# Kernel optimization log

Measured on AMD Instinct MI355X. Metric: run time of the kernel, lower is better.

Reference implementation:

```python
import jax, jax.numpy as jnp
import numpy as np

B, L, D, H, DFF = 4, 2048, 1024, 16, 4096
DH = D // H
INF = 1e12


def setup_inputs() -> dict:
    key = jax.random.key(0)
    ks = jax.random.split(key, 20)
    s = lambda fan_in: 1.0 / np.sqrt(fan_in)
    inp = {
        'x': jax.random.normal(ks[0], (B, L, D), jnp.float32),
        'mask': jax.random.bernoulli(ks[1], 0.1, (B, 1, 1, L)),
        'wq': jax.random.normal(ks[2], (D, D), jnp.float32) * s(D),
        'bq': jnp.zeros((D,), jnp.float32),
        'wk': jax.random.normal(ks[3], (D, D), jnp.float32) * s(D),
        'bk': jnp.zeros((D,), jnp.float32),
        'wv': jax.random.normal(ks[4], (D, D), jnp.float32) * s(D),
        'bv': jnp.zeros((D,), jnp.float32),
        'wo': jax.random.normal(ks[5], (D, D), jnp.float32) * s(D),
        'bo': jnp.zeros((D,), jnp.float32),
        'w1': jax.random.normal(ks[6], (D, DFF), jnp.float32) * s(D),
        'b1': jnp.zeros((DFF,), jnp.float32),
        'w2': jax.random.normal(ks[7], (DFF, D), jnp.float32) * s(DFF),
        'b2': jnp.zeros((D,), jnp.float32),
        'g1': jnp.ones((D,), jnp.float32),
        'beta1': jnp.zeros((D,), jnp.float32),
        'g2': jnp.ones((D,), jnp.float32),
        'beta2': jnp.zeros((D,), jnp.float32),
    }
    return inp


def _layernorm(x, g, b, eps=1e-5):
    mu = jnp.mean(x, axis=-1, keepdims=True)
    var = jnp.mean(jnp.square(x - mu), axis=-1, keepdims=True)
    return (x - mu) * jax.lax.rsqrt(var + eps) * g + b


def reference(x, mask, wq, bq, wk, bk, wv, bv, wo, bo, w1, b1, w2, b2, g1, beta1, g2, beta2):
    # --- self attention ---
    def split_heads(t):  # [B,L,D] -> [B,H,L,DH]
        return t.reshape(B, L, H, DH).transpose(0, 2, 1, 3)

    Q = split_heads(x @ wq + bq)
    K = split_heads(x @ wk + bk)
    V = split_heads(x @ wv + bv)

    dots = jnp.einsum('bhqd,bhkd->bhqk', Q, K) / np.sqrt(DH)  # [B,H,L,L]
    dots = jnp.where(mask, -INF, dots)
    attn = jax.nn.softmax(dots, axis=-1)
    out = jnp.einsum('bhqk,bhkd->bhqd', attn, V)
    out = out.transpose(0, 2, 1, 3).reshape(B, L, D)
    out = out @ wo + bo

    x = _layernorm(x + out, g1, beta1)

    # --- feed forward ---
    h = jax.nn.relu(x @ w1 + b1)
    ff = h @ w2 + b2
    x = _layernorm(x + ff, g2, beta2)
    return x
```

## Files before the change

kernel.cpp:

```cpp
#include <hip/hip_runtime.h>
#include <hip/hip_bf16.h>

#define B_   4
#define L_   2048
#define D_   1024
#define H_   16
#define DH_  64
#define DFF_ 4096
#define M_   (B_ * L_)

typedef __attribute__((ext_vector_type(8))) short bf16x8;
typedef __attribute__((ext_vector_type(4))) float f32x4;

#define GLOAD16(gp, lp)                                                       \
  __builtin_amdgcn_global_load_lds(                                           \
      (const __attribute__((address_space(1))) unsigned int*)(gp),            \
      (__attribute__((address_space(3))) unsigned int*)(lp), 16, 0, 0)

#if __has_builtin(__builtin_amdgcn_exp2f)
#define EXP2F(x) __builtin_amdgcn_exp2f(x)
#else
#define EXP2F(x) exp2f(x)
#endif

__global__ void mask_mode_detect(const unsigned int* __restrict__ m,
                                 int* __restrict__ mode) {
  __shared__ int flags[2];
  if (threadIdx.x < 2) flags[threadIdx.x] = 0;
  __syncthreads();
  int nf32 = 0, n01 = 0;
  for (int i = threadIdx.x; i < 2048; i += 256) {
    unsigned w = m[i];
    if (w != 0u && w != 0x3f800000u) nf32 = 1;
    if (w > 1u) n01 = 1;
  }
  if (nf32) atomicOr(&flags[0], 1);
  if (n01)  atomicOr(&flags[1], 1);
  __syncthreads();
  if (threadIdx.x == 0)
    *mode = (!flags[0]) ? 0 : ((!flags[1]) ? 1 : 2);
}

__global__ void mask_prep(const void* __restrict__ m,
                          const int* __restrict__ mode_p,
                          float* __restrict__ out, int n) {
  int i = blockIdx.x * 256 + threadIdx.x;
  if (i >= n) return;
  int mode = *mode_p;
  bool mk;
  if (mode == 0)      mk = reinterpret_cast<const float*>(m)[i] != 0.f;
  else if (mode == 1) mk = reinterpret_cast<const int*>(m)[i] != 0;
  else                mk = reinterpret_cast<const unsigned char*>(m)[i] != 0;
  out[i] = mk ? -1e12f : 0.f;
}

__global__ void cvt_f32_bf16(const float4* __restrict__ in,
                             ushort4* __restrict__ out, int n4) {
  int i = blockIdx.x * 256 + threadIdx.x;
  if (i >= n4) return;
  float4 v = in[i];
  __hip_bfloat16 a = __float2bfloat16(v.x);
  __hip_bfloat16 b = __float2bfloat16(v.y);
  __hip_bfloat16 c = __float2bfloat16(v.z);
  __hip_bfloat16 d = __float2bfloat16(v.w);
  ushort4 o;
  o.x = *reinterpret_cast<unsigned short*>(&a);
  o.y = *reinterpret_cast<unsigned short*>(&b);
  o.z = *reinterpret_cast<unsigned short*>(&c);
  o.w = *reinterpret_cast<unsigned short*>(&d);
  out[i] = o;
}

__global__ void transpose_cvt(const float* __restrict__ W,
                              __hip_bfloat16* __restrict__ Wt, int K, int N) {
  __shared__ float t[32][33];
  const int n0 = blockIdx.x * 32, k0 = blockIdx.y * 32;
  const int tx = threadIdx.x, ty = threadIdx.y;
#pragma unroll
  for (int i = 0; i < 4; ++i)
    t[ty + i * 8][tx] = W[(size_t)(k0 + ty + i * 8) * N + n0 + tx];
  __syncthreads();
#pragma unroll
  for (int i = 0; i < 4; ++i)
    Wt[(size_t)(n0 + ty + i * 8) * K + k0 + tx] =
        __float2bfloat16(t[tx][ty + i * 8]);
}

__global__ void transpose_v(const __hip_bfloat16* __restrict__ Vin,
                            __hip_bfloat16* __restrict__ Vt) {
  __shared__ __hip_bfloat16 t[32][33];
  const int l0 = blockIdx.x * 32, d0 = blockIdx.y * 32, b = blockIdx.z;
  const int tx = threadIdx.x, ty = threadIdx.y;
#pragma unroll
  for (int i = 0; i < 4; ++i)
    t[ty + i * 8][tx] = Vin[(size_t)(b * L_ + l0 + ty + i * 8) * D_ + d0 + tx];
  __syncthreads();
#pragma unroll
  for (int i = 0; i < 4; ++i) {
    int d = d0 + ty + i * 8;
    Vt[(size_t)(b * D_ + d) * L_ + l0 + tx] = t[tx][ty + i * 8];
  }
}

#define STAGE8(matptr, ldsbase, tile, kh, rowbase)                            \
  {                                                                           \
    _Pragma("unroll")                                                         \
    for (int j_ = 0; j_ < 2; ++j_) {                                          \
      const int s_ = j_ * 512 + tid;                                          \
      const int row_ = s_ >> 2;                                               \
      const int q_ = (s_ & 3) ^ ((row_ >> 1) & 3);                            \
      GLOAD16(&matptr[(size_t)((rowbase) + row_) * K + (tile) * 64 +          \
                      (kh) * 32 + q_ * 8],                                    \
              (ldsbase) + (j_ * 512 + (w << 6)) * 16);                        \
    }                                                                         \
  }

#define PHASE8(bufoff, rh, ks, dovm, ...)                                     \
  {                                                                           \
    if ((rh) == 0) {                                                          \
      _Pragma("unroll")                                                       \
      for (int j = 0; j < 4; ++j) {                                           \
        const int br = wn * 64 + j * 16 + r16;                                \
        bfr[j] = *reinterpret_cast<const bf16x8*>(                            \
            ldsB + (bufoff) + (ks) * 16384 + br * 64 +                        \
            ((hi * 16) ^ (((br >> 1) & 3) << 4)));                            \
      }                                                                       \
    }                                                                         \
    bf16x8 af[4];                                                             \
    _Pragma("unroll")                                                         \
    for (int i = 0; i < 4; ++i) {                                             \
      const int ar = wm * 128 + (rh) * 64 + i * 16 + r16;                     \
      af[i] = *reinterpret_cast<const bf16x8*>(                               \
          ldsA + (bufoff) + (ks) * 16384 + ar * 64 +                          \
          ((hi * 16) ^ (((ar >> 1) & 3) << 4)));                              \
    }                                                                         \
    __VA_ARGS__;                                                              \
    __builtin_amdgcn_s_barrier();                                             \
    asm volatile("s_waitcnt lgkmcnt(0)" ::: "memory");                        \
    __builtin_amdgcn_sched_barrier(0);                                        \
    __builtin_amdgcn_s_setprio(1);                                            \
    _Pragma("unroll")                                                         \
    for (int i = 0; i < 4; ++i)                                               \
      _Pragma("unroll")                                                       \
      for (int j = 0; j < 4; ++j)                                             \
        acc[(rh) * 4 + i][j] = __builtin_amdgcn_mfma_f32_16x16x32_bf16(       \
            af[i], bfr[j], acc[(rh) * 4 + i][j], 0, 0, 0);                    \
    __builtin_amdgcn_s_setprio(0);                                            \
    if (dovm) {                                                               \
      asm volatile("s_waitcnt vmcnt(4)" ::: "memory");                        \
      __builtin_amdgcn_sched_barrier(0);                                      \
    }                                                                         \
    __builtin_amdgcn_s_barrier();                                             \
  }

template <int EP>
__global__ __launch_bounds__(512, 1) void gemm8(
    const __hip_bfloat16* __restrict__ A, const __hip_bfloat16* __restrict__ Bt,
    const float* __restrict__ bias, void* __restrict__ out,
    int M, int N, int K) {
  __shared__ __align__(16) char lds8[131072];
  char* const ldsA = lds8;
  char* const ldsB = lds8 + 65536;

  const int tid = threadIdx.x;
  const int lane = tid & 63;
  const int w = tid >> 6;
  const int wm = w >> 2;
  const int wn = w & 3;
  const int r16 = lane & 15;
  const int hi = lane >> 4;

  const int nwg = gridDim.x;
  const int orig = blockIdx.x;
  const int swz = (orig & 7) * (nwg >> 3) + (orig >> 3);
  const int bm = (swz & 31) * 256;
  const int bn = (swz >> 5) * 256;

  f32x4 acc[8][4];
#pragma unroll
  for (int i = 0; i < 8; ++i)
#pragma unroll
    for (int j = 0; j < 4; ++j) acc[i][j] = (f32x4){0.f, 0.f, 0.f, 0.f};
  bf16x8 bfr[4];

  const int nkt = K >> 6;
  const int nit = nkt >> 1;

  STAGE8(A, ldsA, 0, 0, bm);
  STAGE8(Bt, ldsB, 0, 0, bn);
  STAGE8(A, ldsA + 16384, 0, 1, bm);
  STAGE8(Bt, ldsB + 16384, 0, 1, bn);
  STAGE8(A, ldsA + 32768, 1, 0, bm);
  STAGE8(Bt, ldsB + 32768, 1, 0, bn);
  asm volatile("s_waitcnt vmcnt(4)" ::: "memory");
  __builtin_amdgcn_sched_barrier(0);
  __builtin_amdgcn_s_barrier();

  for (int it = 0; it < nit; ++it) {
    const int kt = it * 2;
    const bool hn = (it + 1) < nit;
    PHASE8(0, 0, 0, 0, STAGE8(A, ldsA + 49152, kt + 1, 1, bm));
    PHASE8(0, 1, 0, 0, STAGE8(Bt, ldsB + 49152, kt + 1, 1, bn));
    PHASE8(0, 0, 1, 0, if (hn) STAGE8(A, ldsA, kt + 2, 0, bm));
    PHASE8(0, 1, 1, 1, if (hn) STAGE8(Bt, ldsB, kt + 2, 0, bn));
    PHASE8(32768, 0, 0, 0, if (hn) STAGE8(A, ldsA + 16384, kt + 2, 1, bm));
    PHASE8(32768, 1, 0, 0, if (hn) STAGE8(Bt, ldsB + 16384, kt + 2, 1, bn));
    PHASE8(32768, 0, 1, 0, if (hn) STAGE8(A, ldsA + 32768, kt + 3, 0, bm));
    PHASE8(32768, 1, 1, 1, if (hn) STAGE8(Bt, ldsB + 32768, kt + 3, 0, bn));
  }

#pragma unroll
  for (int ri = 0; ri < 8; ++ri) {
#pragma unroll
    for (int j = 0; j < 4; ++j) {
      const int col = bn + wn * 64 + j * 16 + r16;
      const float bv = bias[col];
#pragma unroll
      for (int r = 0; r < 4; ++r) {
        const int row = bm + wm * 128 + ri * 16 + hi * 4 + r;
        const float v = acc[ri][j][r] + bv;
        if (EP == 1) {
          ((__hip_bfloat16*)out)[(size_t)row * N + col] =
              __float2bfloat16(v > 0.f ? v : 0.f);
        } else {
          __hip_bfloat16* outp =
              (__hip_bfloat16*)out + (size_t)(col >> 10) * (M_ * D_);
          outp[(size_t)row * 1024 + (col & 1023)] = __float2bfloat16(v);
        }
      }
    }
  }
}

template <int EP>
__global__ __launch_bounds__(256) void gemm_bt(
    const __hip_bfloat16* __restrict__ A, const __hip_bfloat16* __restrict__ Bt,
    const float* __restrict__ bias, const float* __restrict__ res,
    void* __restrict__ out, int M, int N, int K) {
  __shared__ __align__(16) char As[128 * 64];
  __shared__ __align__(16) char Bs[128 * 64];
  const int tid = threadIdx.x;
  const int lane = tid & 63;
  const int w = tid >> 6;
  const int wm = w >> 1, wn = w & 1;
  const int bm = blockIdx.x * 128;
  const int bn = blockIdx.y * 128;
  const int r16 = lane & 15;
  const int hi = lane >> 4;

  f32x4 acc[4][4];
#pragma unroll
  for (int m = 0; m < 4; ++m)
#pragma unroll
    for (int n = 0; n < 4; ++n) acc[m][n] = (f32x4){0.f, 0.f, 0.f, 0.f};

  for (int k0 = 0; k0 < K; k0 += 32) {
    __syncthreads();
#pragma unroll
    for (int c = 0; c < 2; ++c) {
      const int seg = c * 256 + tid;
      const int row = seg >> 2;
      const int csl = (seg & 3) ^ (row & 3);
      GLOAD16(&A[(size_t)(bm + row) * K + k0 + csl * 8],
              As + (c * 256 + w * 64) * 16);
      GLOAD16(&Bt[(size_t)(bn + row) * K + k0 + csl * 8],
              Bs + (c * 256 + w * 64) * 16);
    }
    __syncthreads();

    bf16x8 af[4], bfr[4];
#pragma unroll
    for (int m = 0; m < 4; ++m) {
      const int arow = wm * 64 + m * 16 + r16;
      af[m] = *reinterpret_cast<const bf16x8*>(
          As + arow * 64 + ((hi * 16) ^ ((arow & 3) << 4)));
    }
#pragma unroll
    for (int n = 0; n < 4; ++n) {
      const int brow = wn * 64 + n * 16 + r16;
      bfr[n] = *reinterpret_cast<const bf16x8*>(
          Bs + brow * 64 + ((hi * 16) ^ ((brow & 3) << 4)));
    }
#pragma unroll
    for (int m = 0; m < 4; ++m)
#pragma unroll
      for (int n = 0; n < 4; ++n)
        acc[m][n] = __builtin_amdgcn_mfma_f32_16x16x32_bf16(af[m], bfr[n],
                                                            acc[m][n], 0, 0, 0);
  }

  const int rg = hi * 4;
#pragma unroll
  for (int m = 0; m < 4; ++m) {
#pragma unroll
    for (int n = 0; n < 4; ++n) {
      const int col = bn + wn * 64 + n * 16 + r16;
      const float bv = bias[col];
#pragma unroll
      for (int r = 0; r < 4; ++r) {
        const int row = bm + wm * 64 + m * 16 + rg + r;
        const size_t idx = (size_t)row * N + col;
        float v = acc[m][n][r] + bv;
        if (EP == 0) {
          ((__hip_bfloat16*)out)[idx] = __float2bfloat16(v);
        } else if (EP == 1) {
          ((__hip_bfloat16*)out)[idx] = __float2bfloat16(v > 0.f ? v : 0.f);
        } else {
          ((float*)out)[idx] = v + res[idx];
        }
      }
    }
  }
}

__global__ __launch_bounds__(256) void attn_kernel(
    const __hip_bfloat16* __restrict__ Qg, const __hip_bfloat16* __restrict__ Kg,
    const __hip_bfloat16* __restrict__ VTg,
    const float* __restrict__ maskf,
    __hip_bfloat16* __restrict__ Og) {
  __shared__ __align__(16) char Kl[64 * 128];
  __shared__ __align__(16) char Vl[64 * 128];
  __shared__ __align__(16) char Pl[4][32 * 128];
  __shared__ float maskb[64];

  const int tid = threadIdx.x;
  const int lane = tid & 63;
  const int w = tid >> 6;
  const int hi = lane >> 4;
  const int r16 = lane & 15;
  const int swzk = (r16 & 7) << 4;

  const int nwg = gridDim.x;
  const int orig = blockIdx.x;
  const int swb = (orig & 7) * (nwg >> 3) + (orig >> 3);
  const int qb = swb & 15;
  const int bh = swb >> 4;
  const int b = bh >> 4;
  const int h = bh & 15;
  const int qbase = qb * 128 + w * 32;

  const float C = 0.18033688011112042f;

  bf16x8 qf[2][2];
#pragma unroll
  for (int m = 0; m < 2; ++m)
#pragma unroll
    for (int ks = 0; ks < 2; ++ks)
      qf[m][ks] = *reinterpret_cast<const bf16x8*>(
          &Qg[(size_t)(b * L_ + qbase + m * 16 + r16) * D_ + h * DH_ +
              ks * 32 + hi * 8]);

  float mrun[2] = {-1e30f, -1e30f};
  float lrun[2] = {0.f, 0.f};
  f32x4 o[2][4];
#pragma unroll
  for (int m = 0; m < 2; ++m)
#pragma unroll
    for (int nd = 0; nd < 4; ++nd) o[m][nd] = (f32x4){0.f, 0.f, 0.f, 0.f};

  char* const Plw = Pl[w];

  for (int kv0 = 0; kv0 < L_; kv0 += 64) {
    __syncthreads();
#pragma unroll
    for (int c = 0; c < 2; ++c) {
      const int seg = c * 256 + tid;
      const int row = seg >> 3;
      const int csl = (seg & 7) ^ (row & 7);
      GLOAD16(&Kg[(size_t)(b * L_ + kv0 + row) * D_ + h * DH_ + csl * 8],
              Kl + (c * 256 + w * 64) * 16);
      GLOAD16(&VTg[(size_t)(b * D_ + h * DH_ + row) * L_ + kv0 + csl * 8],
              Vl + (c * 256 + w * 64) * 16);
    }
    if (tid < 64) maskb[tid] = maskf[(size_t)b * L_ + kv0 + tid];
    __syncthreads();

    f32x4 sacc[2][4];
#pragma unroll
    for (int m = 0; m < 2; ++m)
#pragma unroll
      for (int n = 0; n < 4; ++n) sacc[m][n] = (f32x4){0.f, 0.f, 0.f, 0.f};
    __builtin_amdgcn_s_setprio(1);
#pragma unroll
    for (int n = 0; n < 4; ++n) {
      const int krow = n * 16 + r16;
#pragma unroll
      for (int ks = 0; ks < 2; ++ks) {
        const bf16x8 kf = *reinterpret_cast<const bf16x8*>(
            Kl + krow * 128 + ((ks * 64 + hi * 16) ^ swzk));
#pragma unroll
        for (int m = 0; m < 2; ++m)
          sacc[m][n] = __builtin_amdgcn_mfma_f32_16x16x32_bf16(
              kf, qf[m][ks], sacc[m][n], 0, 0, 0);
      }
    }
    __builtin_amdgcn_s_setprio(0);

#pragma unroll
    for (int m = 0; m < 2; ++m) {
      float p[4][4];
#pragma unroll
      for (int n = 0; n < 4; ++n) {
        const float4 mv =
            *reinterpret_cast<const float4*>(&maskb[n * 16 + hi * 4]);
        p[n][0] = fmaf(sacc[m][n][0], C, mv.x);
        p[n][1] = fmaf(sacc[m][n][1], C, mv.y);
        p[n][2] = fmaf(sacc[m][n][2], C, mv.z);
        p[n][3] = fmaf(sacc[m][n][3], C, mv.w);
      }
      float lm = p[0][0];
#pragma unroll
      for (int n = 0; n < 4; ++n)
#pragma unroll
        for (int r = 0; r < 4; ++r) lm = fmaxf(lm, p[n][r]);
      lm = fmaxf(lm, __shfl_xor(lm, 16, 64));
      lm = fmaxf(lm, __shfl_xor(lm, 32, 64));
      if (!__all(lm <= mrun[m] + 8.f)) {
        const float mn = fmaxf(mrun[m], lm);
        const float corr = EXP2F(mrun[m] - mn);
        mrun[m] = mn;
        lrun[m] *= corr;
        float crs[4];
#pragma unroll
        for (int r = 0; r < 4; ++r)
          crs[r] = __shfl(corr, (lane & 48) | (hi * 4 + r), 64);
#pragma unroll
        for (int nd = 0; nd < 4; ++nd)
#pragma unroll
          for (int r = 0; r < 4; ++r) o[m][nd][r] *= crs[r];
      }
      const float mr = mrun[m];
      float ls = 0.f;
      const int prow = m * 16 + r16;
#pragma unroll
      for (int n = 0; n < 4; ++n) {
        union { unsigned long long u; unsigned short us[4]; } pk;
#pragma unroll
        for (int r = 0; r < 4; ++r) {
          const float e = EXP2F(p[n][r] - mr);
          ls += e;
          __hip_bfloat16 t = __float2bfloat16(e);
          pk.us[r] = *reinterpret_cast<unsigned short*>(&t);
        }
        *reinterpret_cast<unsigned long long*>(
            Plw + prow * 128 + ((n * 32 + hi * 8) ^ swzk)) = pk.u;
      }
      lrun[m] += ls;
    }

    bf16x8 pa[2][2];
#pragma unroll
    for (int m = 0; m < 2; ++m)
#pragma unroll
      for (int ks = 0; ks < 2; ++ks)
        pa[m][ks] = *reinterpret_cast<const bf16x8*>(
            Plw + (m * 16 + r16) * 128 + ((ks * 64 + hi * 16) ^ swzk));
    __builtin_amdgcn_s_setprio(1);
#pragma unroll
    for (int nd = 0; nd < 4; ++nd) {
      const int vrow = nd * 16 + r16;
#pragma unroll
      for (int ks = 0; ks < 2; ++ks) {
        const bf16x8 vb = *reinterpret_cast<const bf16x8*>(
            Vl + vrow * 128 + ((ks * 64 + hi * 16) ^ swzk));
#pragma unroll
        for (int m = 0; m < 2; ++m)
          o[m][nd] = __builtin_amdgcn_mfma_f32_16x16x32_bf16(pa[m][ks], vb,
                                                             o[m][nd], 0, 0, 0);
      }
    }
    __builtin_amdgcn_s_setprio(0);
  }

#pragma unroll
  for (int m = 0; m < 2; ++m) {
    lrun[m] += __shfl_xor(lrun[m], 16, 64);
    lrun[m] += __shfl_xor(lrun[m], 32, 64);
    const float inv = 1.f / lrun[m];
    float invr[4];
#pragma unroll
    for (int r = 0; r < 4; ++r)
      invr[r] = __shfl(inv, (lane & 48) | (hi * 4 + r), 64);
#pragma unroll
    for (int r = 0; r < 4; ++r) {
      const int q = qbase + m * 16 + hi * 4 + r;
#pragma unroll
      for (int nd = 0; nd < 4; ++nd)
        Og[(size_t)(b * L_ + q) * D_ + h * DH_ + nd * 16 + r16] =
            __float2bfloat16(o[m][nd][r] * invr[r]);
    }
  }
}

__global__ __launch_bounds__(256) void layernorm_kernel(
    const float* __restrict__ in, const float* __restrict__ g,
    const float* __restrict__ be, float* __restrict__ outf,
    __hip_bfloat16* __restrict__ outb) {
  const int row = blockIdx.x;
  const int tid = threadIdx.x;
  const float4 v = reinterpret_cast<const float4*>(in + (size_t)row * D_)[tid];
  float s = v.x + v.y + v.z + v.w;
  float ss = v.x * v.x + v.y * v.y + v.z * v.z + v.w * v.w;
#pragma unroll
  for (int off = 1; off < 64; off <<= 1) {
    s += __shfl_xor(s, off, 64);
    ss += __shfl_xor(ss, off, 64);
  }
  __shared__ float red[8];
  const int w = tid >> 6, lane = tid & 63;
  if (lane == 0) { red[w] = s; red[4 + w] = ss; }
  __syncthreads();
  s = red[0] + red[1] + red[2] + red[3];
  ss = red[4] + red[5] + red[6] + red[7];
  const float mu = s * (1.f / D_);
  const float rs = rsqrtf(ss * (1.f / D_) - mu * mu + 1e-5f);
  const float4 gv = reinterpret_cast<const float4*>(g)[tid];
  const float4 bv = reinterpret_cast<const float4*>(be)[tid];
  float4 ov;
  ov.x = (v.x - mu) * rs * gv.x + bv.x;
  ov.y = (v.y - mu) * rs * gv.y + bv.y;
  ov.z = (v.z - mu) * rs * gv.z + bv.z;
  ov.w = (v.w - mu) * rs * gv.w + bv.w;
  reinterpret_cast<float4*>(outf + (size_t)row * D_)[tid] = ov;
  if (outb) {
    __hip_bfloat16 t[4] = {__float2bfloat16(ov.x), __float2bfloat16(ov.y),
                           __float2bfloat16(ov.z), __float2bfloat16(ov.w)};
    *reinterpret_cast<uint2*>(&outb[(size_t)row * D_ + tid * 4]) =
        *reinterpret_cast<const uint2*>(t);
  }
}

extern "C" void kernel_launch(void* const* d_in, const int* in_sizes, int n_in,
                              void* d_out, int out_size, void* d_ws,
                              size_t ws_size, hipStream_t stream) {
  (void)in_sizes; (void)n_in; (void)out_size; (void)ws_size;
  const float* x   = (const float*)d_in[0];
  const void*  msk = d_in[1];
  const float* wq  = (const float*)d_in[2];
  const float* bq  = (const float*)d_in[3];
  const float* wk  = (const float*)d_in[4];
  const float* bk  = (const float*)d_in[5];
  const float* wv  = (const float*)d_in[6];
  const float* bv  = (const float*)d_in[7];
  const float* wo  = (const float*)d_in[8];
  const float* bo  = (const float*)d_in[9];
  const float* w1  = (const float*)d_in[10];
  const float* b1  = (const float*)d_in[11];
  const float* w2  = (const float*)d_in[12];
  const float* b2  = (const float*)d_in[13];
  const float* g1  = (const float*)d_in[14];
  const float* be1 = (const float*)d_in[15];
  const float* g2  = (const float*)d_in[16];
  const float* be2 = (const float*)d_in[17];

  char* ws = (char*)d_ws;
  int*            MODE  = (int*)(ws + 0);
  float*          MASKF = (float*)(ws + 256);
  float*          BIASC = (float*)(ws + 40960);
  __hip_bfloat16* XB    = (__hip_bfloat16*)(ws + 65536);
  __hip_bfloat16* WQT   = (__hip_bfloat16*)(ws + 16842752);
  __hip_bfloat16* WKT   = (__hip_bfloat16*)(ws + 18939904);
  __hip_bfloat16* WVT   = (__hip_bfloat16*)(ws + 21037056);
  __hip_bfloat16* WOT   = (__hip_bfloat16*)(ws + 23134208);
  __hip_bfloat16* W1T   = (__hip_bfloat16*)(ws + 25231360);
  __hip_bfloat16* W2T   = (__hip_bfloat16*)(ws + 33619968);
  __hip_bfloat16* QB    = (__hip_bfloat16*)(ws + 42008576);
  __hip_bfloat16* KB    = (__hip_bfloat16*)(ws + 58785792);
  __hip_bfloat16* VB    = (__hip_bfloat16*)(ws + 75563008);
  __hip_bfloat16* OB    = (__hip_bfloat16*)(ws + 92340224);
  __hip_bfloat16* HB    = QB;
  __hip_bfloat16* VT    = (__hip_bfloat16*)(ws + 109117440);
  float*          R1    = (float*)(ws + 125894656);
  float*          OUT   = (float*)d_out;

  mask_mode_detect<<<1, 256, 0, stream>>>((const unsigned int*)msk, MODE);
  mask_prep<<<(B_ * L_ + 255) / 256, 256, 0, stream>>>(msk, MODE, MASKF, B_ * L_);
  cvt_f32_bf16<<<(M_ * D_ / 4 + 255) / 256, 256, 0, stream>>>(
      (const float4*)x, (ushort4*)XB, M_ * D_ / 4);
  hipMemcpyAsync(BIASC, bq, D_ * 4, hipMemcpyDeviceToDevice, stream);
  hipMemcpyAsync(BIASC + D_, bk, D_ * 4, hipMemcpyDeviceToDevice, stream);
  hipMemcpyAsync(BIASC + 2 * D_, bv, D_ * 4, hipMemcpyDeviceToDevice, stream);

  dim3 tb(32, 8);
  transpose_cvt<<<dim3(D_ / 32, D_ / 32), tb, 0, stream>>>(wq, WQT, D_, D_);
  transpose_cvt<<<dim3(D_ / 32, D_ / 32), tb, 0, stream>>>(wk, WKT, D_, D_);
  transpose_cvt<<<dim3(D_ / 32, D_ / 32), tb, 0, stream>>>(wv, WVT, D_, D_);
  transpose_cvt<<<dim3(D_ / 32, D_ / 32), tb, 0, stream>>>(wo, WOT, D_, D_);
  transpose_cvt<<<dim3(DFF_ / 32, D_ / 32), tb, 0, stream>>>(w1, W1T, D_, DFF_);
  transpose_cvt<<<dim3(D_ / 32, DFF_ / 32), tb, 0, stream>>>(w2, W2T, DFF_, D_);

  gemm8<3><<<dim3((M_ / 256) * (3 * D_ / 256)), 512, 0, stream>>>(
      XB, WQT, BIASC, QB, M_, 3 * D_, D_);

  transpose_v<<<dim3(L_ / 32, D_ / 32, B_), tb, 0, stream>>>(VB, VT);
  attn_kernel<<<dim3(B_ * H_ * (L_ / 128)), 256, 0, stream>>>(QB, KB, VT, MASKF, OB);

  gemm_bt<2><<<dim3(M_ / 128, D_ / 128), 256, 0, stream>>>(OB, WOT, bo, x, R1, M_, D_, D_);
  layernorm_kernel<<<M_, 256, 0, stream>>>(R1, g1, be1, R1, XB);
  gemm8<1><<<dim3((M_ / 256) * (DFF_ / 256)), 512, 0, stream>>>(
      XB, W1T, b1, HB, M_, DFF_, D_);
  gemm_bt<2><<<dim3(M_ / 128, D_ / 128), 256, 0, stream>>>(HB, W2T, b2, R1, OUT, M_, D_, DFF_);
  layernorm_kernel<<<M_, 256, 0, stream>>>(OUT, g2, be2, OUT, nullptr);
}
```

Measured before the change: 490.1 us.

## Split-K the FFN down-projection on the large GEMM kernel and fuse combine with LayerNorm

The second FFN GEMM (K=4096, N=1024) now runs on the 256x256 gemm8 kernel with a 2-way split over K, which gives 256 workgroups instead of 128. Each half writes an fp32 partial, and a new combine_ln2 kernel sums both partials with the residual and bias before applying LayerNorm. This replaces the smaller 128-tile gemm_bt plus a separate layernorm pass. The attention row-max reduction is also rewritten as a tree. The cost is about 64MB of extra fp32 partial traffic, and the path only runs if the workspace is large enough.

```diff
diff --git a/kernel.cpp b/kernel.cpp
--- a/kernel.cpp
+++ b/kernel.cpp
@@ -102,14 +102,14 @@
   }
 }
 
-#define STAGE8(matptr, ldsbase, tile, kh, rowbase)                            \
+#define STAGE8(matptr, stride, ldsbase, tile, kh, rowbase)                    \
   {                                                                           \
     _Pragma("unroll")                                                         \
     for (int j_ = 0; j_ < 2; ++j_) {                                          \
       const int s_ = j_ * 512 + tid;                                          \
       const int row_ = s_ >> 2;                                               \
       const int q_ = (s_ & 3) ^ ((row_ >> 1) & 3);                            \
-      GLOAD16(&matptr[(size_t)((rowbase) + row_) * K + (tile) * 64 +          \
+      GLOAD16(&matptr[(size_t)((rowbase) + row_) * (stride) + (tile) * 64 +   \
                       (kh) * 32 + q_ * 8],                                    \
               (ldsbase) + (j_ * 512 + (w << 6)) * 16);                        \
     }                                                                         \
@@ -157,7 +157,7 @@
 __global__ __launch_bounds__(512, 1) void gemm8(
     const __hip_bfloat16* __restrict__ A, const __hip_bfloat16* __restrict__ Bt,
     const float* __restrict__ bias, void* __restrict__ out,
-    int M, int N, int K) {
+    int M, int N, int K, int lda, int ldb) {
   __shared__ __align__(16) char lds8[131072];
   char* const ldsA = lds8;
   char* const ldsB = lds8 + 65536;
@@ -173,8 +173,21 @@
   const int nwg = gridDim.x;
   const int orig = blockIdx.x;
   const int swz = (orig & 7) * (nwg >> 3) + (orig >> 3);
-  const int bm = (swz & 31) * 256;
-  const int bn = (swz >> 5) * 256;
+
+  int bm, bn, kh = 0;
+  const __hip_bfloat16* Ap = A;
+  const __hip_bfloat16* Bp = Bt;
+  if (EP == 4) {
+    kh = swz & 1;
+    const int rest = swz >> 1;
+    bm = (rest & 31) * 256;
+    bn = (rest >> 5) * 256;
+    Ap += (size_t)kh * K;
+    Bp += (size_t)kh * K;
+  } else {
+    bm = (swz & 31) * 256;
+    bn = (swz >> 5) * 256;
+  }
 
   f32x4 acc[8][4];
 #pragma unroll
@@ -186,12 +199,12 @@
   const int nkt = K >> 6;
   const int nit = nkt >> 1;
 
-  STAGE8(A, ldsA, 0, 0, bm);
-  STAGE8(Bt, ldsB, 0, 0, bn);
-  STAGE8(A, ldsA + 16384, 0, 1, bm);
-  STAGE8(Bt, ldsB + 16384, 0, 1, bn);
-  STAGE8(A, ldsA + 32768, 1, 0, bm);
-  STAGE8(Bt, ldsB + 32768, 1, 0, bn);
+  STAGE8(Ap, lda, ldsA, 0, 0, bm);
+  STAGE8(Bp, ldb, ldsB, 0, 0, bn);
+  STAGE8(Ap, lda, ldsA + 16384, 0, 1, bm);
+  STAGE8(Bp, ldb, ldsB + 16384, 0, 1, bn);
+  STAGE8(Ap, lda, ldsA + 32768, 1, 0, bm);
+  STAGE8(Bp, ldb, ldsB + 32768, 1, 0, bn);
   asm volatile("s_waitcnt vmcnt(4)" ::: "memory");
   __builtin_amdgcn_sched_barrier(0);
   __builtin_amdgcn_s_barrier();
@@ -199,14 +212,14 @@
   for (int it = 0; it < nit; ++it) {
     const int kt = it * 2;
     const bool hn = (it + 1) < nit;
-    PHASE8(0, 0, 0, 0, STAGE8(A, ldsA + 49152, kt + 1, 1, bm));
-    PHASE8(0, 1, 0, 0, STAGE8(Bt, ldsB + 49152, kt + 1, 1, bn));
-    PHASE8(0, 0, 1, 0, if (hn) STAGE8(A, ldsA, kt + 2, 0, bm));
-    PHASE8(0, 1, 1, 1, if (hn) STAGE8(Bt, ldsB, kt + 2, 0, bn));
-    PHASE8(32768, 0, 0, 0, if (hn) STAGE8(A, ldsA + 16384, kt + 2, 1, bm));
-    PHASE8(32768, 1, 0, 0, if (hn) STAGE8(Bt, ldsB + 16384, kt + 2, 1, bn));
-    PHASE8(32768, 0, 1, 0, if (hn) STAGE8(A, ldsA + 32768, kt + 3, 0, bm));
-    PHASE8(32768, 1, 1, 1, if (hn) STAGE8(Bt, ldsB + 32768, kt + 3, 0, bn));
+    PHASE8(0, 0, 0, 0, STAGE8(Ap, lda, ldsA + 49152, kt + 1, 1, bm));
+    PHASE8(0, 1, 0, 0, STAGE8(Bp, ldb, ldsB + 49152, kt + 1, 1, bn));
+    PHASE8(0, 0, 1, 0, if (hn) STAGE8(Ap, lda, ldsA, kt + 2, 0, bm));
+    PHASE8(0, 1, 1, 1, if (hn) STAGE8(Bp, ldb, ldsB, kt + 2, 0, bn));
+    PHASE8(32768, 0, 0, 0, if (hn) STAGE8(Ap, lda, ldsA + 16384, kt + 2, 1, bm));
+    PHASE8(32768, 1, 0, 0, if (hn) STAGE8(Bp, ldb, ldsB + 16384, kt + 2, 1, bn));
+    PHASE8(32768, 0, 1, 0, if (hn) STAGE8(Ap, lda, ldsA + 32768, kt + 3, 0, bm));
+    PHASE8(32768, 1, 1, 1, if (hn) STAGE8(Bp, ldb, ldsB + 32768, kt + 3, 0, bn));
   }
 
 #pragma unroll
@@ -214,7 +227,7 @@
 #pragma unroll
     for (int j = 0; j < 4; ++j) {
       const int col = bn + wn * 64 + j * 16 + r16;
-      const float bv = bias[col];
+      const float bv = (EP == 4) ? 0.f : bias[col];
 #pragma unroll
       for (int r = 0; r < 4; ++r) {
         const int row = bm + wm * 128 + ri * 16 + hi * 4 + r;
@@ -222,10 +235,13 @@
         if (EP == 1) {
           ((__hip_bfloat16*)out)[(size_t)row * N + col] =
               __float2bfloat16(v > 0.f ? v : 0.f);
-        } else {
+        } else if (EP == 3) {
           __hip_bfloat16* outp =
               (__hip_bfloat16*)out + (size_t)(col >> 10) * (M_ * D_);
           outp[(size_t)row * 1024 + (col & 1023)] = __float2bfloat16(v);
+        } else {
+          float* outp = (float*)out + (size_t)kh * ((size_t)M * N);
+          outp[(size_t)row * N + col] = v;
         }
       }
     }
@@ -408,11 +424,11 @@
         p[n][2] = fmaf(sacc[m][n][2], C, mv.z);
         p[n][3] = fmaf(sacc[m][n][3], C, mv.w);
       }
-      float lm = p[0][0];
-#pragma unroll
-      for (int n = 0; n < 4; ++n)
-#pragma unroll
-        for (int r = 0; r < 4; ++r) lm = fmaxf(lm, p[n][r]);
+      float q0 = fmaxf(fmaxf(p[0][0], p[0][1]), fmaxf(p[0][2], p[0][3]));
+      float q1 = fmaxf(fmaxf(p[1][0], p[1][1]), fmaxf(p[1][2], p[1][3]));
+      float q2 = fmaxf(fmaxf(p[2][0], p[2][1]), fmaxf(p[2][2], p[2][3]));
+      float q3 = fmaxf(fmaxf(p[3][0], p[3][1]), fmaxf(p[3][2], p[3][3]));
+      float lm = fmaxf(fmaxf(q0, q1), fmaxf(q2, q3));
       lm = fmaxf(lm, __shfl_xor(lm, 16, 64));
       lm = fmaxf(lm, __shfl_xor(lm, 32, 64));
       if (!__all(lm <= mrun[m] + 8.f)) {
@@ -530,10 +546,51 @@
   }
 }
 
+__global__ __launch_bounds__(256) void combine_ln2(
+    const float* __restrict__ P0, const float* __restrict__ P1,
+    const float* __restrict__ res, const float* __restrict__ b2,
+    const float* __restrict__ g, const float* __restrict__ be,
+    float* __restrict__ out) {
+  const int row = blockIdx.x;
+  const int tid = threadIdx.x;
+  const float4 a = reinterpret_cast<const float4*>(P0 + (size_t)row * D_)[tid];
+  const float4 b = reinterpret_cast<const float4*>(P1 + (size_t)row * D_)[tid];
+  const float4 rr = reinterpret_cast<const float4*>(res + (size_t)row * D_)[tid];
+  const float4 bb = reinterpret_cast<const float4*>(b2)[tid];
+  float4 v;
+  v.x = a.x + b.x + rr.x + bb.x;
+  v.y = a.y + b.y + rr.y + bb.y;
+  v.z = a.z + b.z + rr.z + bb.z;
+  v.w = a.w + b.w + rr.w + bb.w;
+  float s = v.x + v.y + v.z + v.w;
+  float ss = v.x * v.x + v.y * v.y + v.z * v.z + v.w * v.w;
+#pragma unroll
+  for (int off = 1; off < 64; off <<= 1) {
+    s += __shfl_xor(s, off, 64);
+    ss += __shfl_xor(ss, off, 64);
+  }
+  __shared__ float red[8];
+  const int w = tid >> 6, lane = tid & 63;
+  if (lane == 0) { red[w] = s; red[4 + w] = ss; }
+  __syncthreads();
+  s = red[0] + red[1] + red[2] + red[3];
+  ss = red[4] + red[5] + red[6] + red[7];
+  const float mu = s * (1.f / D_);
+  const float rs = rsqrtf(ss * (1.f / D_) - mu * mu + 1e-5f);
+  const float4 gv = reinterpret_cast<const float4*>(g)[tid];
+  const float4 bv = reinterpret_cast<const float4*>(be)[tid];
+  float4 ov;
+  ov.x = (v.x - mu) * rs * gv.x + bv.x;
+  ov.y = (v.y - mu) * rs * gv.y + bv.y;
+  ov.z = (v.z - mu) * rs * gv.z + bv.z;
+  ov.w = (v.w - mu) * rs * gv.w + bv.w;
+  reinterpret_cast<float4*>(out + (size_t)row * D_)[tid] = ov;
+}
+
 extern "C" void kernel_launch(void* const* d_in, const int* in_sizes, int n_in,
                               void* d_out, int out_size, void* d_ws,
                               size_t ws_size, hipStream_t stream) {
-  (void)in_sizes; (void)n_in; (void)out_size; (void)ws_size;
+  (void)in_sizes; (void)n_in; (void)out_size;
   const float* x   = (const float*)d_in[0];
   const void*  msk = d_in[1];
   const float* wq  = (const float*)d_in[2];
@@ -571,7 +628,10 @@
   __hip_bfloat16* HB    = QB;
   __hip_bfloat16* VT    = (__hip_bfloat16*)(ws + 109117440);
   float*          R1    = (float*)(ws + 125894656);
+  float*          P0    = (float*)(ws + 159449088);
+  float*          P1    = (float*)(ws + 193003520);
   float*          OUT   = (float*)d_out;
+  const bool use_splitk = ws_size >= 226557952ull;
 
   mask_mode_detect<<<1, 256, 0, stream>>>((const unsigned int*)msk, MODE);
   mask_prep<<<(B_ * L_ + 255) / 256, 256, 0, stream>>>(msk, MODE, MASKF, B_ * L_);
@@ -590,7 +650,7 @@
   transpose_cvt<<<dim3(D_ / 32, DFF_ / 32), tb, 0, stream>>>(w2, W2T, DFF_, D_);
 
   gemm8<3><<<dim3((M_ / 256) * (3 * D_ / 256)), 512, 0, stream>>>(
-      XB, WQT, BIASC, QB, M_, 3 * D_, D_);
+      XB, WQT, BIASC, QB, M_, 3 * D_, D_, D_, D_);
 
   transpose_v<<<dim3(L_ / 32, D_ / 32, B_), tb, 0, stream>>>(VB, VT);
   attn_kernel<<<dim3(B_ * H_ * (L_ / 128)), 256, 0, stream>>>(QB, KB, VT, MASKF, OB);
@@ -598,7 +658,13 @@
   gemm_bt<2><<<dim3(M_ / 128, D_ / 128), 256, 0, stream>>>(OB, WOT, bo, x, R1, M_, D_, D_);
   layernorm_kernel<<<M_, 256, 0, stream>>>(R1, g1, be1, R1, XB);
   gemm8<1><<<dim3((M_ / 256) * (DFF_ / 256)), 512, 0, stream>>>(
-      XB, W1T, b1, HB, M_, DFF_, D_);
-  gemm_bt<2><<<dim3(M_ / 128, D_ / 128), 256, 0, stream>>>(HB, W2T, b2, R1, OUT, M_, D_, DFF_);
-  layernorm_kernel<<<M_, 256, 0, stream>>>(OUT, g2, be2, OUT, nullptr);
-}
+      XB, W1T, b1, HB, M_, DFF_, D_, D_, D_);
+  if (use_splitk) {
+    gemm8<4><<<dim3((M_ / 256) * (D_ / 256) * 2), 512, 0, stream>>>(
+        HB, W2T, nullptr, P0, M_, D_, DFF_ / 2, DFF_, DFF_);
+    combine_ln2<<<M_, 256, 0, stream>>>(P0, P1, R1, b2, g2, be2, OUT);
+  } else {
+    gemm_bt<2><<<dim3(M_ / 128, D_ / 128), 256, 0, stream>>>(HB, W2T, b2, R1, OUT, M_, D_, DFF_);
+    layernorm_kernel<<<M_, 256, 0, stream>>>(OUT, g2, be2, OUT, nullptr);
+  }
+}
```

Result: faster. 474.3 us (-3.2%).
